# Kernel tuning notes

Hardware: AMD Instinct MI355X
Metric: run time of the kernel (lower is better)

## Reference

```python
import jax, jax.numpy as jnp
import numpy as np

B, T, N, K, d = 8, 12, 325, 8, 64
D = K * d


def setup_inputs() -> dict:
    key = jax.random.key(0)
    ks = jax.random.split(key, 12)
    s = 0.02
    f32 = jnp.float32
    inp = {
        "X": jax.random.normal(ks[0], (B, T, N, D), f32),
        "STE": jax.random.normal(ks[1], (B, T, N, D), f32),
        "Wq": (jax.random.normal(ks[2], (2 * D, D), f32) * s),
        "bq": jnp.zeros((D,), f32),
        "Wk": (jax.random.normal(ks[3], (2 * D, D), f32) * s),
        "bk": jnp.zeros((D,), f32),
        "Wv": (jax.random.normal(ks[4], (2 * D, D), f32) * s),
        "bv": jnp.zeros((D,), f32),
        "W1": (jax.random.normal(ks[5], (D, D), f32) * s),
        "b1": jnp.zeros((D,), f32),
        "W2": (jax.random.normal(ks[6], (D, D), f32) * s),
        "b2": jnp.zeros((D,), f32),
        "attn_mask": 0,
    }
    return inp


def reference(X, STE, Wq, bq, Wk, bk, Wv, bv, W1, b1, W2, b2, attn_mask):
    # X, STE: [B, T, N, D]
    Xc = jnp.concatenate([X, STE], axis=-1)          # [B,T,N,2D]
    q = jax.nn.relu(Xc @ Wq + bq).reshape(B, T, N, K, d)
    k = jax.nn.relu(Xc @ Wk + bk).reshape(B, T, N, K, d)
    v = jax.nn.relu(Xc @ Wv + bv).reshape(B, T, N, K, d)

    # scores: [B, K, T, N, N] (attention over spatial/node axis N)
    scores = jnp.einsum('btnhe,btmhe->bhtnm', q, k)
    # mask_flag=False -> TriangularCausalMask applied (upper-tri masked with -inf)
    causal = jnp.triu(jnp.ones((N, N), dtype=bool), 1)
    scores = jnp.where(causal, -jnp.inf, scores)
    # original scales AFTER masking; -inf / sqrt(d) stays -inf
    scores = scores / jnp.sqrt(jnp.asarray(d, scores.dtype))
    attn = jax.nn.softmax(scores, axis=-1)
    # dropout: eval mode (identity)

    ctx = jnp.einsum('bhtnm,btmhe->btnhe', attn, v).reshape(B, T, N, D)
    out = jax.nn.relu(ctx @ W1 + b1) @ W2 + b2        # [B,T,N,D]

    # match torch's head-major cat(dim=0): [K*B, T, N, N]
    attn_full = jnp.transpose(attn, (1, 0, 2, 3, 4)).reshape(K * B, T, N, N)
    return out, attn_full
```

## Files before the change

kernel.cpp:

```cpp
#include <hip/hip_runtime.h>
#include <hip/hip_bf16.h>

typedef __hip_bfloat16 bf16;
using f32x4  = __attribute__((ext_vector_type(4))) float;
using short8 = __attribute__((ext_vector_type(8))) short;

#define M_ROWS   31200
#define M_PAD    31232
#define N_TOK    325
#define D_MODEL  512
#define QKV_LD   1536

#define GLOBAL_AS(p) ((const __attribute__((address_space(1))) unsigned int*)(p))
#define LDS_AS(p)    ((__attribute__((address_space(3))) unsigned int*)(p))

__global__ void init_flag(int* flag) { if (threadIdx.x == 0) *flag = 0; }

__global__ void detect_dtype(const unsigned short* __restrict__ x, int* flag)
{
    int i = blockIdx.x * 256 + threadIdx.x;
    unsigned short h = x[i];
    int e = (h >> 7) & 0xFF;
    if (e >= 135) atomicOr(flag, 1);
}

__device__ __forceinline__ float load_in(const void* p, size_t i, bool f32)
{
    return f32 ? ((const float*)p)[i] : __bfloat162float(((const bf16*)p)[i]);
}

__global__ void concat_cast(const void* __restrict__ X, const void* __restrict__ STE,
                            bf16* __restrict__ Xc, const int* __restrict__ flag)
{
    const bool f32 = (*flag != 0);
    int idx = blockIdx.x * 256 + threadIdx.x;
    int r = idx >> 7, c8 = (idx & 127) << 3;
    short8 v = {0, 0, 0, 0, 0, 0, 0, 0};
    if (r < M_ROWS) {
        const void* src = (c8 < 512) ? X : STE;
        int cc = c8 & 511;
        if (f32) {
            const float* s = (const float*)src + (size_t)r * 512 + cc;
            float4 a = *(const float4*)s;
            float4 b = *(const float4*)(s + 4);
            ((bf16*)&v)[0] = __float2bfloat16(a.x); ((bf16*)&v)[1] = __float2bfloat16(a.y);
            ((bf16*)&v)[2] = __float2bfloat16(a.z); ((bf16*)&v)[3] = __float2bfloat16(a.w);
            ((bf16*)&v)[4] = __float2bfloat16(b.x); ((bf16*)&v)[5] = __float2bfloat16(b.y);
            ((bf16*)&v)[6] = __float2bfloat16(b.z); ((bf16*)&v)[7] = __float2bfloat16(b.w);
        } else {
            v = *(const short8*)((const bf16*)src + (size_t)r * 512 + cc);
        }
    }
    *(short8*)&Xc[(size_t)r * 1024 + c8] = v;
}

__global__ void transpose_w_tiled(const void* __restrict__ src, bf16* __restrict__ dst,
                                  int krows, int ncols, const int* __restrict__ flag)
{
    __shared__ float tile[32][33];
    const bool f32 = (*flag != 0);
    const int kt = blockIdx.y * 32, nt = blockIdx.x * 32;
    const int tx = threadIdx.x & 31, ty = threadIdx.x >> 5;
#pragma unroll
    for (int r = 0; r < 32; r += 8)
        tile[ty + r][tx] = load_in(src, (size_t)(kt + ty + r) * ncols + (nt + tx), f32);
    __syncthreads();
#pragma unroll
    for (int r = 0; r < 32; r += 8)
        dst[(size_t)(nt + ty + r) * krows + (kt + tx)] = __float2bfloat16(tile[tx][ty + r]);
}

__global__ void prep_bias(const void* __restrict__ bq, const void* __restrict__ bk,
                          const void* __restrict__ bv, const void* __restrict__ b1,
                          const void* __restrict__ b2,
                          float* __restrict__ biasQKV, float* __restrict__ b1f,
                          float* __restrict__ b2f, const int* __restrict__ flag)
{
    const bool f32 = (*flag != 0);
    int i = blockIdx.x * 256 + threadIdx.x;
    if (i < 512) {
        biasQKV[i]        = load_in(bq, i, f32);
        biasQKV[512 + i]  = load_in(bk, i, f32);
        biasQKV[1024 + i] = load_in(bv, i, f32);
        b1f[i] = load_in(b1, i, f32);
        b2f[i] = load_in(b2, i, f32);
    }
}

template<int OUTF32>
__global__ __launch_bounds__(256) void gemm_lds(
    const bf16* __restrict__ A, int lda,
    const bf16* __restrict__ Bt, int ldb,
    const float* __restrict__ bias, void* __restrict__ Cv,
    int Mvalid, int Kdim, int ldc, int do_relu, int nby)
{
    __shared__ alignas(16) bf16 As0[128 * 32];
    __shared__ alignas(16) bf16 As1[128 * 32];
    __shared__ alignas(16) bf16 Bs0[128 * 32];
    __shared__ alignas(16) bf16 Bs1[128 * 32];
    const int cpx = gridDim.x >> 3;
    const int swz = (blockIdx.x & 7) * cpx + (blockIdx.x >> 3);
    const int m0 = (swz / nby) * 128;
    const int n0 = (swz % nby) * 128;
    const int t = threadIdx.x, wave = t >> 6, lane = t & 63;
    const int wm = (wave >> 1) * 64, wn = (wave & 1) * 64;
    const int lrow = lane & 15, lk8 = (lane >> 4) * 8;
    const int srow = lane >> 2, scol = (lane & 3) << 3;
    f32x4 acc[4][4] = {};
    const int nk = Kdim >> 6;

    for (int ks = 0; ks < nk; ++ks) {
        const int kk = ks << 6;
        __syncthreads();
#pragma unroll
        for (int c = 0; c < 2; ++c) {
            const int chunk = wave * 2 + c;
            const bf16* ga = A  + (size_t)(m0 + chunk * 16 + srow) * lda + kk + scol;
            const bf16* gb = Bt + (size_t)(n0 + chunk * 16 + srow) * ldb + kk + scol;
            __builtin_amdgcn_global_load_lds(GLOBAL_AS(ga),      LDS_AS(As0 + chunk * 512), 16, 0, 0);
            __builtin_amdgcn_global_load_lds(GLOBAL_AS(ga + 32), LDS_AS(As1 + chunk * 512), 16, 0, 0);
            __builtin_amdgcn_global_load_lds(GLOBAL_AS(gb),      LDS_AS(Bs0 + chunk * 512), 16, 0, 0);
            __builtin_amdgcn_global_load_lds(GLOBAL_AS(gb + 32), LDS_AS(Bs1 + chunk * 512), 16, 0, 0);
        }
        __syncthreads();
        short8 af[4], bfr[4];
#pragma unroll
        for (int i = 0; i < 4; ++i) {
            af[i]  = *(const short8*)&As0[(wm + i * 16 + lrow) * 32 + lk8];
            bfr[i] = *(const short8*)&Bs0[(wn + i * 16 + lrow) * 32 + lk8];
        }
#pragma unroll
        for (int i = 0; i < 4; ++i)
#pragma unroll
            for (int j = 0; j < 4; ++j)
                acc[i][j] = __builtin_amdgcn_mfma_f32_16x16x32_bf16(
                    af[i], bfr[j], acc[i][j], 0, 0, 0);
#pragma unroll
        for (int i = 0; i < 4; ++i) {
            af[i]  = *(const short8*)&As1[(wm + i * 16 + lrow) * 32 + lk8];
            bfr[i] = *(const short8*)&Bs1[(wn + i * 16 + lrow) * 32 + lk8];
        }
#pragma unroll
        for (int i = 0; i < 4; ++i)
#pragma unroll
            for (int j = 0; j < 4; ++j)
                acc[i][j] = __builtin_amdgcn_mfma_f32_16x16x32_bf16(
                    af[i], bfr[j], acc[i][j], 0, 0, 0);
    }

    const int r4 = (lane >> 4) * 4;
#pragma unroll
    for (int i = 0; i < 4; ++i) {
#pragma unroll
        for (int r = 0; r < 4; ++r) {
            int grow = m0 + wm + i * 16 + r4 + r;
            if (OUTF32 && grow >= Mvalid) continue;
#pragma unroll
            for (int j = 0; j < 4; ++j) {
                int gcol = n0 + wn + j * 16 + lrow;
                float v  = acc[i][j][r] + bias[gcol];
                if (do_relu) v = fmaxf(v, 0.0f);
                if (OUTF32)
                    ((float*)Cv)[(size_t)grow * ldc + gcol] = v;
                else
                    ((bf16*)Cv)[(size_t)grow * ldc + gcol] = __float2bfloat16(v);
            }
        }
    }
}

#define KS_LD  72
#define VT_LD  354
__global__ __launch_bounds__(512) void attn_kernel(
    bf16* __restrict__ qkv, float* __restrict__ attn_out)
{
    __shared__ alignas(16) bf16 Ks[336 * KS_LD];
    __shared__ alignas(16) bf16 Vt[64 * VT_LD + 32];
    __shared__ alignas(16) bf16 ptile[8][16 * 40];
    const int t = threadIdx.x, lane = t & 63, w = t >> 6;
    const int h = blockIdx.x & 7, bt = blockIdx.x >> 3;
    const size_t rowbase = (size_t)bt * N_TOK;
    const int lrow = lane & 15, lk8 = (lane >> 4) * 8;
    const int r4 = (lane >> 4) * 4;
    const int b = bt / 12, tt2 = bt % 12;
    const size_t hb_base = (((size_t)(h * 8 + b)) * 12 + tt2) * N_TOK;

    for (int task = t; task < 336 * 8; task += 512) {
        int m = task >> 3, e0 = (task & 7) << 3;
        short8 v = {0, 0, 0, 0, 0, 0, 0, 0};
        if (m < N_TOK)
            v = *(const short8*)(qkv + (rowbase + m) * QKV_LD + 512 + h * 64 + e0);
        *(short8*)&Ks[m * KS_LD + e0] = v;
    }
    for (int task = t; task < 352 * 8; task += 512) {
        int m = task >> 3, e0 = (task & 7) << 3;
        short8 v = {0, 0, 0, 0, 0, 0, 0, 0};
        if (m < N_TOK)
            v = *(const short8*)(qkv + (rowbase + m) * QKV_LD + 1024 + h * 64 + e0);
#pragma unroll
        for (int j = 0; j < 8; ++j)
            Vt[(e0 + j) * VT_LD + m] = ((bf16*)&v)[j];
    }
    __syncthreads();

    for (int it = 0; it < 3; ++it) {
        if (it == 2 && w > 4) break;
        const int tile = (it < 2) ? (w + it * 8) : (20 - w);
        const int r0 = tile * 16;

        int qrow = r0 + lrow; if (qrow > N_TOK - 1) qrow = N_TOK - 1;
        const bf16* qp = qkv + (rowbase + qrow) * QKV_LD + h * 64 + lk8;
        short8 qa0 = *(const short8*)(qp);
        short8 qa1 = *(const short8*)(qp + 32);

        f32x4 f[22];
        f[21] = (f32x4){0.f, 0.f, 0.f, 0.f};
#pragma unroll
        for (int ct = 0; ct < 21; ++ct) {
            if (ct <= tile) {
                f32x4 a = {0.f, 0.f, 0.f, 0.f};
                short8 kb0 = *(const short8*)&Ks[(ct * 16 + lrow) * KS_LD + lk8];
                short8 kb1 = *(const short8*)&Ks[(ct * 16 + lrow) * KS_LD + 32 + lk8];
                a = __builtin_amdgcn_mfma_f32_16x16x32_bf16(qa0, kb0, a, 0, 0, 0);
                a = __builtin_amdgcn_mfma_f32_16x16x32_bf16(qa1, kb1, a, 0, 0, 0);
                f[ct] = a;
            }
        }

        float mx[4] = {-1e30f, -1e30f, -1e30f, -1e30f};
        float sm[4] = {0.f, 0.f, 0.f, 0.f};
#pragma unroll
        for (int ct = 0; ct < 21; ++ct) {
            if (ct <= tile) {
                const int c = ct * 16 + lrow;
#pragma unroll
                for (int r = 0; r < 4; ++r)
                    if (c <= r0 + r4 + r) mx[r] = fmaxf(mx[r], f[ct][r]);
            }
        }
#pragma unroll
        for (int r = 0; r < 4; ++r) {
#pragma unroll
            for (int o = 1; o < 16; o <<= 1) mx[r] = fmaxf(mx[r], __shfl_xor(mx[r], o));
        }
#pragma unroll
        for (int ct = 0; ct < 21; ++ct) {
            if (ct <= tile) {
                const int c = ct * 16 + lrow;
#pragma unroll
                for (int r = 0; r < 4; ++r) {
                    float e = (c <= r0 + r4 + r)
                                  ? __expf((f[ct][r] - mx[r]) * 0.125f) : 0.f;
                    f[ct][r] = e;
                    sm[r] += e;
                }
            }
        }
#pragma unroll
        for (int r = 0; r < 4; ++r) {
#pragma unroll
            for (int o = 1; o < 16; o <<= 1) sm[r] += __shfl_xor(sm[r], o);
            sm[r] = 1.0f / sm[r];
        }
#pragma unroll
        for (int ct = 0; ct < 21; ++ct) {
            if (ct <= tile) {
#pragma unroll
                for (int r = 0; r < 4; ++r) f[ct][r] *= sm[r];
            }
        }

#pragma unroll
        for (int ct = 0; ct < 21; ++ct) {
            const int c = ct * 16 + lrow;
            if (c < N_TOK) {
#pragma unroll
                for (int r = 0; r < 4; ++r) {
                    const int n = r0 + r4 + r;
                    if (n < N_TOK) {
                        float v = (ct <= tile && c <= n) ? f[ct][r] : 0.f;
                        attn_out[(hb_base + n) * N_TOK + c] = v;
                    }
                }
            }
        }

        f32x4 acc[4] = {};
        bf16* pt = &ptile[w][0];
#pragma unroll
        for (int s = 0; s < 11; ++s) {
            if (s <= (tile >> 1)) {
#pragma unroll
                for (int half = 0; half < 2; ++half) {
                    const int ct2 = 2 * s + half;
                    const int c = ct2 * 16 + lrow;
#pragma unroll
                    for (int r = 0; r < 4; ++r) {
                        const int n = r0 + r4 + r;
                        float v = (ct2 <= tile && c <= n) ? f[ct2][r] : 0.f;
                        pt[(r4 + r) * 40 + half * 16 + lrow] = __float2bfloat16(v);
                    }
                }
                short8 aa = *(const short8*)&pt[lrow * 40 + lk8];
#pragma unroll
                for (int e = 0; e < 4; ++e) {
                    short8 bb = *(const short8*)&Vt[(e * 16 + lrow) * VT_LD + s * 32 + lk8];
                    acc[e] = __builtin_amdgcn_mfma_f32_16x16x32_bf16(aa, bb, acc[e], 0, 0, 0);
                }
            }
        }

#pragma unroll
        for (int e = 0; e < 4; ++e) {
#pragma unroll
            for (int r = 0; r < 4; ++r) {
                const int n = r0 + r4 + r;
                if (n < N_TOK)
                    qkv[(rowbase + n) * QKV_LD + h * 64 + e * 16 + lrow] =
                        __float2bfloat16(acc[e][r]);
            }
        }
    }
}

extern "C" void kernel_launch(void* const* d_in, const int* in_sizes, int n_in,
                              void* d_out, int out_size, void* d_ws, size_t ws_size,
                              hipStream_t stream)
{
    const void* X   = d_in[0];
    const void* STE = d_in[1];
    const void* Wq  = d_in[2];
    const void* bq  = d_in[3];
    const void* Wk  = d_in[4];
    const void* bk  = d_in[5];
    const void* Wv  = d_in[6];
    const void* bv  = d_in[7];
    const void* W1  = d_in[8];
    const void* b1  = d_in[9];
    const void* W2  = d_in[10];
    const void* b2  = d_in[11];

    float* out0     = (float*)d_out;
    float* attn_out = (float*)d_out + (size_t)M_ROWS * D_MODEL;
    bf16*  Xc       = (bf16*)attn_out;

    char* ws = (char*)d_ws;
    bf16*  qkv   = (bf16*)(ws);
    bf16*  BtQKV = (bf16*)(ws + 95944704);
    bf16*  W1T   = (bf16*)(ws + 99090432);
    bf16*  W2T   = (bf16*)(ws + 99614720);
    float* biasQ = (float*)(ws + 100139008);
    float* b1f   = (float*)(ws + 100145152);
    float* b2f   = (float*)(ws + 100147200);
    int*   flag  = (int*)(ws + 100149248);
    bf16*  hbuf  = qkv + 512;

    init_flag<<<1, 64, 0, stream>>>(flag);
    detect_dtype<<<64, 256, 0, stream>>>((const unsigned short*)X, flag);

    transpose_w_tiled<<<dim3(16, 32), 256, 0, stream>>>(Wq, BtQKV, 1024, 512, flag);
    transpose_w_tiled<<<dim3(16, 32), 256, 0, stream>>>(Wk, BtQKV + 512 * 1024, 1024, 512, flag);
    transpose_w_tiled<<<dim3(16, 32), 256, 0, stream>>>(Wv, BtQKV + 1024 * 1024, 1024, 512, flag);
    transpose_w_tiled<<<dim3(16, 16), 256, 0, stream>>>(W1, W1T, 512, 512, flag);
    transpose_w_tiled<<<dim3(16, 16), 256, 0, stream>>>(W2, W2T, 512, 512, flag);
    prep_bias<<<2, 256, 0, stream>>>(bq, bk, bv, b1, b2, biasQ, b1f, b2f, flag);

    concat_cast<<<(M_PAD * 128) / 256, 256, 0, stream>>>(X, STE, Xc, flag);

    gemm_lds<0><<<244 * 12, 256, 0, stream>>>(
        Xc, 1024, BtQKV, 1024, biasQ, qkv, M_PAD, 1024, QKV_LD, 1, 12);

    attn_kernel<<<768, 512, 0, stream>>>(qkv, attn_out);

    gemm_lds<0><<<244 * 4, 256, 0, stream>>>(
        qkv, QKV_LD, W1T, 512, b1f, hbuf, M_PAD, 512, QKV_LD, 1, 4);

    gemm_lds<1><<<244 * 4, 256, 0, stream>>>(
        hbuf, QKV_LD, W2T, 512, b2f, out0, M_ROWS, 512, D_MODEL, 0, 4);
}
```

Before: 419.8 us.

## Use 256x128 GEMM tiles and precompute transposed V in global memory

Widens the GEMM block tile from 128x128 to 256x128 with 512 threads. Each B tile is reused across twice as many rows, and the grid is halved. Adds a separate vt_transpose kernel that writes V transposed and zero-padded into scratch space in the output buffer. The attention kernel then reads V fragments straight from global memory instead of transposing into LDS with scalar stores, freeing LDS. The trade-off is an extra kernel launch, extra global traffic, and uncached global reads in the inner PV loop.

Result: no change. 422.5 us (+0.7%).

```diff
diff --git a/kernel.cpp b/kernel.cpp
--- a/kernel.cpp
+++ b/kernel.cpp
@@ -10,6 +10,7 @@
 #define N_TOK    325
 #define D_MODEL  512
 #define QKV_LD   1536
+#define VTG_LD   336
 
 #define GLOBAL_AS(p) ((const __attribute__((address_space(1))) unsigned int*)(p))
 #define LDS_AS(p)    ((__attribute__((address_space(3))) unsigned int*)(p))
@@ -87,20 +88,39 @@
     }
 }
 
-template<int OUTF32>
-__global__ __launch_bounds__(256) void gemm_lds(
+__global__ void vt_transpose(const bf16* __restrict__ qkv, bf16* __restrict__ vtg)
+{
+    __shared__ bf16 vs[N_TOK * 72];
+    const int t = threadIdx.x;
+    const int h = blockIdx.x & 7, bt = blockIdx.x >> 3;
+    const size_t rowbase = (size_t)bt * N_TOK;
+    for (int task = t; task < N_TOK * 8; task += 256) {
+        int m = task >> 3, e0 = (task & 7) << 3;
+        *(short8*)&vs[m * 72 + e0] =
+            *(const short8*)(qkv + (rowbase + m) * QKV_LD + 1024 + h * 64 + e0);
+    }
+    __syncthreads();
+    bf16* dst = vtg + (size_t)blockIdx.x * 64 * VTG_LD;
+    for (int task = t; task < 64 * VTG_LD; task += 256) {
+        int e = task / VTG_LD, m = task % VTG_LD;
+        dst[task] = (m < N_TOK) ? vs[m * 72 + e] : __float2bfloat16(0.f);
+    }
+}
+
+template<int OUTF32, int RELU>
+__global__ __launch_bounds__(512) void gemm_lds256(
     const bf16* __restrict__ A, int lda,
     const bf16* __restrict__ Bt, int ldb,
     const float* __restrict__ bias, void* __restrict__ Cv,
-    int Mvalid, int Kdim, int ldc, int do_relu, int nby)
-{
-    __shared__ alignas(16) bf16 As0[128 * 32];
-    __shared__ alignas(16) bf16 As1[128 * 32];
+    int Mvalid, int Kdim, int ldc, int nby)
+{
+    __shared__ alignas(16) bf16 As0[256 * 32];
+    __shared__ alignas(16) bf16 As1[256 * 32];
     __shared__ alignas(16) bf16 Bs0[128 * 32];
     __shared__ alignas(16) bf16 Bs1[128 * 32];
     const int cpx = gridDim.x >> 3;
     const int swz = (blockIdx.x & 7) * cpx + (blockIdx.x >> 3);
-    const int m0 = (swz / nby) * 128;
+    const int m0 = (swz / nby) * 256;
     const int n0 = (swz % nby) * 128;
     const int t = threadIdx.x, wave = t >> 6, lane = t & 63;
     const int wm = (wave >> 1) * 64, wn = (wave & 1) * 64;
@@ -114,13 +134,16 @@
         __syncthreads();
 #pragma unroll
         for (int c = 0; c < 2; ++c) {
-            const int chunk = wave * 2 + c;
-            const bf16* ga = A  + (size_t)(m0 + chunk * 16 + srow) * lda + kk + scol;
-            const bf16* gb = Bt + (size_t)(n0 + chunk * 16 + srow) * ldb + kk + scol;
-            __builtin_amdgcn_global_load_lds(GLOBAL_AS(ga),      LDS_AS(As0 + chunk * 512), 16, 0, 0);
-            __builtin_amdgcn_global_load_lds(GLOBAL_AS(ga + 32), LDS_AS(As1 + chunk * 512), 16, 0, 0);
-            __builtin_amdgcn_global_load_lds(GLOBAL_AS(gb),      LDS_AS(Bs0 + chunk * 512), 16, 0, 0);
-            __builtin_amdgcn_global_load_lds(GLOBAL_AS(gb + 32), LDS_AS(Bs1 + chunk * 512), 16, 0, 0);
+            const int arow = wave * 32 + c * 16;
+            const bf16* ga = A + (size_t)(m0 + arow + srow) * lda + kk + scol;
+            __builtin_amdgcn_global_load_lds(GLOBAL_AS(ga),      LDS_AS(As0 + arow * 32), 16, 0, 0);
+            __builtin_amdgcn_global_load_lds(GLOBAL_AS(ga + 32), LDS_AS(As1 + arow * 32), 16, 0, 0);
+        }
+        {
+            const int brow = wave * 16;
+            const bf16* gb = Bt + (size_t)(n0 + brow + srow) * ldb + kk + scol;
+            __builtin_amdgcn_global_load_lds(GLOBAL_AS(gb),      LDS_AS(Bs0 + brow * 32), 16, 0, 0);
+            __builtin_amdgcn_global_load_lds(GLOBAL_AS(gb + 32), LDS_AS(Bs1 + brow * 32), 16, 0, 0);
         }
         __syncthreads();
         short8 af[4], bfr[4];
@@ -159,7 +182,7 @@
             for (int j = 0; j < 4; ++j) {
                 int gcol = n0 + wn + j * 16 + lrow;
                 float v  = acc[i][j][r] + bias[gcol];
-                if (do_relu) v = fmaxf(v, 0.0f);
+                if (RELU) v = fmaxf(v, 0.0f);
                 if (OUTF32)
                     ((float*)Cv)[(size_t)grow * ldc + gcol] = v;
                 else
@@ -170,12 +193,11 @@
 }
 
 #define KS_LD  72
-#define VT_LD  354
 __global__ __launch_bounds__(512) void attn_kernel(
-    bf16* __restrict__ qkv, float* __restrict__ attn_out)
+    bf16* __restrict__ qkv, const bf16* __restrict__ vtg,
+    float* __restrict__ attn_out)
 {
     __shared__ alignas(16) bf16 Ks[336 * KS_LD];
-    __shared__ alignas(16) bf16 Vt[64 * VT_LD + 32];
     __shared__ alignas(16) bf16 ptile[8][16 * 40];
     const int t = threadIdx.x, lane = t & 63, w = t >> 6;
     const int h = blockIdx.x & 7, bt = blockIdx.x >> 3;
@@ -184,6 +206,7 @@
     const int r4 = (lane >> 4) * 4;
     const int b = bt / 12, tt2 = bt % 12;
     const size_t hb_base = (((size_t)(h * 8 + b)) * 12 + tt2) * N_TOK;
+    const bf16* vt = vtg + (size_t)blockIdx.x * 64 * VTG_LD;
 
     for (int task = t; task < 336 * 8; task += 512) {
         int m = task >> 3, e0 = (task & 7) << 3;
@@ -191,15 +214,6 @@
         if (m < N_TOK)
             v = *(const short8*)(qkv + (rowbase + m) * QKV_LD + 512 + h * 64 + e0);
         *(short8*)&Ks[m * KS_LD + e0] = v;
-    }
-    for (int task = t; task < 352 * 8; task += 512) {
-        int m = task >> 3, e0 = (task & 7) << 3;
-        short8 v = {0, 0, 0, 0, 0, 0, 0, 0};
-        if (m < N_TOK)
-            v = *(const short8*)(qkv + (rowbase + m) * QKV_LD + 1024 + h * 64 + e0);
-#pragma unroll
-        for (int j = 0; j < 8; ++j)
-            Vt[(e0 + j) * VT_LD + m] = ((bf16*)&v)[j];
     }
     __syncthreads();
 
@@ -304,7 +318,7 @@
                 short8 aa = *(const short8*)&pt[lrow * 40 + lk8];
 #pragma unroll
                 for (int e = 0; e < 4; ++e) {
-                    short8 bb = *(const short8*)&Vt[(e * 16 + lrow) * VT_LD + s * 32 + lk8];
+                    short8 bb = *(const short8*)&vt[(e * 16 + lrow) * VTG_LD + s * 32 + lk8];
                     acc[e] = __builtin_amdgcn_mfma_f32_16x16x32_bf16(aa, bb, acc[e], 0, 0, 0);
                 }
             }
@@ -343,6 +357,7 @@
     float* out0     = (float*)d_out;
     float* attn_out = (float*)d_out + (size_t)M_ROWS * D_MODEL;
     bf16*  Xc       = (bf16*)attn_out;
+    bf16*  vtg      = (bf16*)d_out;
 
     char* ws = (char*)d_ws;
     bf16*  qkv   = (bf16*)(ws);
@@ -367,14 +382,16 @@
 
     concat_cast<<<(M_PAD * 128) / 256, 256, 0, stream>>>(X, STE, Xc, flag);
 
-    gemm_lds<0><<<244 * 12, 256, 0, stream>>>(
-        Xc, 1024, BtQKV, 1024, biasQ, qkv, M_PAD, 1024, QKV_LD, 1, 12);
-
-    attn_kernel<<<768, 512, 0, stream>>>(qkv, attn_out);
-
-    gemm_lds<0><<<244 * 4, 256, 0, stream>>>(
-        qkv, QKV_LD, W1T, 512, b1f, hbuf, M_PAD, 512, QKV_LD, 1, 4);
-
-    gemm_lds<1><<<244 * 4, 256, 0, stream>>>(
-        hbuf, QKV_LD, W2T, 512, b2f, out0, M_ROWS, 512, D_MODEL, 0, 4);
-}
+    gemm_lds256<0, 1><<<122 * 12, 512, 0, stream>>>(
+        Xc, 1024, BtQKV, 1024, biasQ, qkv, M_PAD, 1024, QKV_LD, 12);
+
+    vt_transpose<<<768, 256, 0, stream>>>(qkv, vtg);
+
+    attn_kernel<<<768, 512, 0, stream>>>(qkv, vtg, attn_out);
+
+    gemm_lds256<0, 1><<<122 * 4, 512, 0, stream>>>(
+        qkv, QKV_LD, W1T, 512, b1f, hbuf, M_PAD, 512, QKV_LD, 4);
+
+    gemm_lds256<1, 0><<<122 * 4, 512, 0, stream>>>(
+        hbuf, QKV_LD, W2T, 512, b2f, out0, M_ROWS, 512, D_MODEL, 4);
+}
```
